# Kernel optimization log

Measured on AMD Instinct MI355X. Metric: run time of the kernel, lower is better.

The kernel has to match this reference:

```python
import jax, jax.numpy as jnp
import numpy as np

LRELU = 0.2


def _gru(x, Wi, Wh, bi, bh):
    # x: [B,T,D]; Wi: [3H,D]; Wh: [3H,H]; PyTorch GRU equations.
    B, T, D = x.shape
    H = Wh.shape[1]
    xW = jnp.einsum('btd,gd->btg', x, Wi) + bi  # precompute input projections
    def step(h, xw):
        gh = h @ Wh.T + bh
        xr, xz, xn = jnp.split(xw, 3, axis=-1)
        hr, hz, hn = jnp.split(gh, 3, axis=-1)
        r = jax.nn.sigmoid(xr + hr)
        z = jax.nn.sigmoid(xz + hz)
        n = jnp.tanh(xn + r * hn)
        h_new = (1.0 - z) * n + z * h
        return h_new, h_new
    h0 = jnp.zeros((B, H), x.dtype)
    hT, hs = jax.lax.scan(step, h0, jnp.swapaxes(xW, 0, 1))
    return jnp.swapaxes(hs, 0, 1), hT


def _gatv2(x, W, b, a, bias):
    # x: [B,N,F]; W: [2F,E]; lin([v_i||v_j]) == x_i@W1 + x_j@W2 + b (avoids materializing concat)
    F = x.shape[-1]
    W1, W2 = W[:F], W[F:]
    g1 = x @ W1            # [B,N,E]
    g2 = x @ W2 + b        # [B,N,E]
    z = jax.nn.leaky_relu(g1[:, :, None, :] + g2[:, None, :, :], LRELU)  # [B,N,N,E]
    e = jnp.einsum('bije,e->bij', z, a) + bias
    att = jax.nn.softmax(e, axis=2)
    return jax.nn.sigmoid(jnp.einsum('bij,bjf->bif', att, x))


def setup_inputs() -> dict:
    B, W, K, H, KS = 16, 256, 64, 150, 7
    key = jax.random.key(0)
    ks = jax.random.split(key, 32)
    def rn(i, sh, scale):
        return jax.random.normal(ks[i], sh, jnp.float32) * scale
    inp = {}
    inp['x'] = jax.random.normal(ks[0], (B, W, K), jnp.float32)
    inp['conv_w'] = rn(1, (K, K, KS), 1.0 / np.sqrt(K * KS))
    inp['conv_b'] = rn(2, (K,), 0.02)
    inp['fW'] = rn(3, (2 * W, 2 * W), 1.0 / np.sqrt(2 * W))
    inp['fb'] = rn(4, (2 * W,), 0.02)
    inp['fa'] = rn(5, (2 * W,), 1.0 / np.sqrt(2 * W))
    inp['fbias'] = rn(6, (K, K), 0.02)
    inp['tW'] = rn(7, (2 * K, 2 * K), 1.0 / np.sqrt(2 * K))
    inp['tb'] = rn(8, (2 * K,), 0.02)
    inp['ta'] = rn(9, (2 * K,), 1.0 / np.sqrt(2 * K))
    inp['tbias'] = rn(10, (W, W), 0.02)
    inp['gWi'] = rn(11, (3 * H, 3 * K), 1.0 / np.sqrt(H))
    inp['gWh'] = rn(12, (3 * H, H), 1.0 / np.sqrt(H))
    inp['gbi'] = rn(13, (3 * H,), 0.02)
    inp['gbh'] = rn(14, (3 * H,), 0.02)
    inp['f0w'] = rn(15, (H, H), 1.0 / np.sqrt(H))
    inp['f0b'] = rn(16, (H,), 0.02)
    inp['f1w'] = rn(17, (H, K), 1.0 / np.sqrt(H))
    inp['f1b'] = rn(18, (K,), 0.02)
    inp['rWi'] = rn(19, (3 * H, H), 1.0 / np.sqrt(H))
    inp['rWh'] = rn(20, (3 * H, H), 1.0 / np.sqrt(H))
    inp['rbi'] = rn(21, (3 * H,), 0.02)
    inp['rbh'] = rn(22, (3 * H,), 0.02)
    inp['rfw'] = rn(23, (H, K), 1.0 / np.sqrt(H))
    inp['rfb'] = rn(24, (K,), 0.02)
    return inp


def reference(x, conv_w, conv_b, fW, fb, fa, fbias, tW, tb, ta, tbias,
              gWi, gWh, gbi, gbh, f0w, f0b, f1w, f1b,
              rWi, rWh, rbi, rbh, rfw, rfb):
    B, Wsz, K = x.shape
    pad = (conv_w.shape[2] - 1) // 2
    # ConvLayer: permute -> constant pad -> conv1d -> relu -> permute back
    x_ncw = jnp.swapaxes(x, 1, 2)  # [B,K,W]
    x_pad = jnp.pad(x_ncw, ((0, 0), (0, 0), (pad, pad)))
    xc = jax.lax.conv_general_dilated(x_pad, conv_w, (1,), 'VALID',
                                      dimension_numbers=('NCW', 'OIW', 'NCW'))
    xc = jax.nn.relu(xc + conv_b[None, :, None])
    xc = jnp.swapaxes(xc, 1, 2)  # [B,W,K]
    # Feature GAT over nodes (K), temporal GAT over time (W)
    h_feat = jnp.swapaxes(_gatv2(jnp.swapaxes(xc, 1, 2), fW, fb, fa, fbias), 1, 2)  # [B,W,K]
    h_temp = _gatv2(xc, tW, tb, ta, tbias)  # [B,W,K]
    h_cat = jnp.concatenate([xc, h_feat, h_temp], axis=2)  # [B,W,3K]
    _, h_end = _gru(h_cat, gWi, gWh, gbi, gbh)  # [B,H]
    # Forecasting MLP (n_layers=1 -> two Linear layers)
    predictions = jax.nn.relu(h_end @ f0w + f0b) @ f1w + f1b  # [B,K]
    # Reconstruction: repeat_interleave over dim 1 then view(B, W, -1)
    H = h_end.shape[1]
    h_rep = jnp.repeat(h_end, Wsz, axis=1).reshape(B, Wsz, H)
    dec_out, _ = _gru(h_rep, rWi, rWh, rbi, rbh)  # [B,W,H]
    recons = dec_out @ rfw + rfb  # [B,W,K]
    return predictions, recons
```

## Files before the change

### kernel.cpp

```cpp
#include <hip/hip_runtime.h>
#include <hip/hip_fp16.h>

typedef _Float16 h2f __attribute__((ext_vector_type(2)));

__device__ __forceinline__ float dot2f(unsigned a, unsigned b, float c) {
#if __has_builtin(__builtin_amdgcn_fdot2)
  return __builtin_amdgcn_fdot2(__builtin_bit_cast(h2f, a),
                                __builtin_bit_cast(h2f, b), c, false);
#else
  h2f x = __builtin_bit_cast(h2f, a);
  h2f y = __builtin_bit_cast(h2f, b);
  return c + (float)x[0] * (float)y[0] + (float)x[1] * (float)y[1];
#endif
}

__device__ __forceinline__ float sigf(float x) { return 1.0f / (1.0f + __expf(-x)); }
__device__ __forceinline__ float tanhfast(float x) {
  float e = __expf(-2.0f * fabsf(x));
  float r = (1.0f - e) / (1.0f + e);
  return (x < 0.0f) ? -r : r;
}
__device__ __forceinline__ float lrelu(float x) { return x > 0.0f ? x : 0.2f * x; }

__global__ void k_prep(const float* __restrict__ conv_w, const float* __restrict__ gWi,
                       const float* __restrict__ gWh, const float* __restrict__ rWh,
                       const float* __restrict__ rWi,
                       float* __restrict__ cwT, float* __restrict__ gWiT,
                       unsigned* __restrict__ gWhP, unsigned* __restrict__ rWhP,
                       float* __restrict__ pref) {
  const int N0 = 64 * 64 * 7;
  const int N1 = 192 * 450;
  const int N2 = 76 * 450;
  const int N3 = 76 * 450;
  const int N4 = 450;
  int total = N0 + N1 + N2 + N3 + N4;
  for (int idx = blockIdx.x * blockDim.x + threadIdx.x; idx < total;
       idx += gridDim.x * blockDim.x) {
    if (idx < N0) {
      int k = idx & 63; int is = idx >> 6; int i = is / 7; int s = is - i * 7;
      cwT[idx] = conv_w[(k * 64 + i) * 7 + s];
    } else if (idx < N0 + N1) {
      int j = idx - N0; int g = j % 450; int d = j / 450;
      gWiT[j] = gWi[g * 192 + d];
    } else if (idx < N0 + N1 + N2) {
      int j = idx - (N0 + N1); int g = j % 450; int jj = j / 450;
      int j0 = 2 * jj, j1 = 2 * jj + 1;
      float a = (j0 < 150) ? gWh[g * 150 + j0] : 0.f;
      float b = (j1 < 150) ? gWh[g * 150 + j1] : 0.f;
      __half2 h = __floats2half2_rn(a, b);
      gWhP[j] = *reinterpret_cast<unsigned*>(&h);
    } else if (idx < N0 + N1 + N2 + N3) {
      int j = idx - (N0 + N1 + N2); int g = j % 450; int jj = j / 450;
      int j0 = 2 * jj, j1 = 2 * jj + 1;
      float a = (j0 < 150) ? rWh[g * 150 + j0] : 0.f;
      float b = (j1 < 150) ? rWh[g * 150 + j1] : 0.f;
      __half2 h = __floats2half2_rn(a, b);
      rWhP[j] = *reinterpret_cast<unsigned*>(&h);
    } else {
      int g = idx - (N0 + N1 + N2 + N3);
      float run = 0.f;
      pref[g] = 0.f;
      for (int j = 0; j < 150; ++j) { run += rWi[g * 150 + j]; pref[(j + 1) * 450 + g] = run; }
    }
  }
}

__global__ __launch_bounds__(256) void k_conv(const float* __restrict__ x,
                                              const float* __restrict__ cwT,
                                              const float* __restrict__ conv_b,
                                              float* __restrict__ xc) {
  __shared__ float xs[22 * 64];
  int b = blockIdx.y, t0 = blockIdx.x * 16, tid = threadIdx.x;
  for (int l = tid; l < 22 * 64; l += 256) {
    int r = l >> 6, i = l & 63;
    int t = t0 - 3 + r;
    xs[l] = (t >= 0 && t < 256) ? x[(b * 256 + t) * 64 + i] : 0.f;
  }
  __syncthreads();
  int k = tid & 63, tg = tid >> 6;
  float bias = conv_b[k];
  float acc[4] = {bias, bias, bias, bias};
  for (int i = 0; i < 64; ++i) {
#pragma unroll
    for (int s = 0; s < 7; ++s) {
      float wv = cwT[(i * 7 + s) * 64 + k];
#pragma unroll
      for (int q = 0; q < 4; ++q)
        acc[q] += xs[(tg * 4 + q + s) * 64 + i] * wv;
    }
  }
#pragma unroll
  for (int q = 0; q < 4; ++q)
    xc[(b * 256 + t0 + tg * 4 + q) * 64 + k] = fmaxf(acc[q], 0.f);
}

__global__ __launch_bounds__(512) void k_featg(const float* __restrict__ xc,
                                               const float* __restrict__ fW,
                                               const float* __restrict__ fb,
                                               float* __restrict__ g1f,
                                               float* __restrict__ g2fT) {
  __shared__ float xsL[256 * 8];
  int b = blockIdx.y, i0 = blockIdx.x * 8, e = threadIdx.x;
  for (int l = e; l < 2048; l += 512) {
    int t = l >> 3, ii = l & 7;
    xsL[l] = xc[(b * 256 + t) * 64 + i0 + ii];
  }
  __syncthreads();
  float a1[8] = {}, a2[8] = {};
  for (int t = 0; t < 256; ++t) {
    float w1 = fW[t * 512 + e];
    float w2 = fW[(256 + t) * 512 + e];
#pragma unroll
    for (int ii = 0; ii < 8; ++ii) {
      float s = xsL[t * 8 + ii];
      a1[ii] += s * w1; a2[ii] += s * w2;
    }
  }
  float fbe = fb[e];
#pragma unroll
  for (int ii = 0; ii < 8; ++ii)
    g1f[(b * 64 + i0 + ii) * 512 + e] = a1[ii];
  float4 v0 = make_float4(a2[0] + fbe, a2[1] + fbe, a2[2] + fbe, a2[3] + fbe);
  float4 v1 = make_float4(a2[4] + fbe, a2[5] + fbe, a2[6] + fbe, a2[7] + fbe);
  float4* p = reinterpret_cast<float4*>(&g2fT[(b * 512 + e) * 64 + i0]);
  p[0] = v0; p[1] = v1;
}

__global__ __launch_bounds__(256) void k_feata(const float* __restrict__ xc,
                                               const float* __restrict__ g1f,
                                               const float* __restrict__ g2fT,
                                               const float* __restrict__ fa,
                                               const float* __restrict__ fbias,
                                               float* __restrict__ h_feat) {
  __shared__ float g1L[512], faL[512], part[4 * 64], attL[64];
  int b = blockIdx.y, i = blockIdx.x, tid = threadIdx.x;
  for (int l = tid; l < 512; l += 256) {
    g1L[l] = g1f[(b * 64 + i) * 512 + l];
    faL[l] = fa[l];
  }
  __syncthreads();
  int q = tid >> 6, j = tid & 63;
  float acc = 0.f;
  for (int e = q * 128; e < q * 128 + 128; ++e) {
    float z = g1L[e] + g2fT[(b * 512 + e) * 64 + j];
    acc += faL[e] * lrelu(z);
  }
  part[q * 64 + j] = acc;
  __syncthreads();
  if (tid < 64) {
    float ev = part[tid] + part[64 + tid] + part[128 + tid] + part[192 + tid] +
               fbias[i * 64 + tid];
    float m = ev;
#pragma unroll
    for (int off = 32; off > 0; off >>= 1) m = fmaxf(m, __shfl_xor(m, off));
    float p = __expf(ev - m);
    float s = p;
#pragma unroll
    for (int off = 32; off > 0; off >>= 1) s += __shfl_xor(s, off);
    attL[tid] = p / s;
  }
  __syncthreads();
  float o = 0.f;
  for (int jj = 0; jj < 64; ++jj)
    o += attL[jj] * xc[(b * 256 + tid) * 64 + jj];
  h_feat[(b * 256 + tid) * 64 + i] = sigf(o);
}

__global__ __launch_bounds__(256) void k_tempg(const float* __restrict__ xc,
                                               const float* __restrict__ tW,
                                               const float* __restrict__ tb,
                                               float* __restrict__ g1t,
                                               float* __restrict__ g2tT) {
  __shared__ float xsL[16 * 64];
  int b = blockIdx.y, t0 = blockIdx.x * 16, tid = threadIdx.x;
  int e = tid & 127, th = tid >> 7;
  for (int l = tid; l < 1024; l += 256)
    xsL[l] = xc[(b * 256 + t0) * 64 + l];
  __syncthreads();
  float a1[8] = {}, a2[8] = {};
  for (int k = 0; k < 64; ++k) {
    float w1 = tW[k * 128 + e];
    float w2 = tW[(64 + k) * 128 + e];
#pragma unroll
    for (int tt = 0; tt < 8; ++tt) {
      float s = xsL[(th * 8 + tt) * 64 + k];
      a1[tt] += s * w1; a2[tt] += s * w2;
    }
  }
  float tbe = tb[e];
#pragma unroll
  for (int tt = 0; tt < 8; ++tt)
    g1t[(b * 256 + t0 + th * 8 + tt) * 128 + e] = a1[tt];
  float4 v0 = make_float4(a2[0] + tbe, a2[1] + tbe, a2[2] + tbe, a2[3] + tbe);
  float4 v1 = make_float4(a2[4] + tbe, a2[5] + tbe, a2[6] + tbe, a2[7] + tbe);
  float4* p = reinterpret_cast<float4*>(&g2tT[(b * 128 + e) * 256 + t0 + th * 8]);
  p[0] = v0; p[1] = v1;
}

__global__ __launch_bounds__(256) void k_tempa(const float* __restrict__ xc,
                                               const float* __restrict__ g1t,
                                               const float* __restrict__ g2tT,
                                               const float* __restrict__ ta,
                                               const float* __restrict__ tbias,
                                               float* __restrict__ h_temp) {
  __shared__ float g1L[4 * 128], taL[128], eL[4 * 256];
  int b = blockIdx.y, i0 = blockIdx.x * 4, tid = threadIdx.x;
  for (int l = tid; l < 512; l += 256)
    g1L[l] = g1t[(b * 256 + i0) * 128 + l];
  if (tid < 128) taL[tid] = ta[tid];
  __syncthreads();
  float acc[4] = {};
  for (int e = 0; e < 128; ++e) {
    float g2 = g2tT[(b * 128 + e) * 256 + tid];
    float tae = taL[e];
#pragma unroll
    for (int ii = 0; ii < 4; ++ii)
      acc[ii] += tae * lrelu(g1L[ii * 128 + e] + g2);
  }
#pragma unroll
  for (int ii = 0; ii < 4; ++ii)
    eL[ii * 256 + tid] = acc[ii] + tbias[(i0 + ii) * 256 + tid];
  __syncthreads();
  int wv = tid >> 6, ln = tid & 63;
  {
    float v0 = eL[wv * 256 + ln], v1 = eL[wv * 256 + 64 + ln];
    float v2 = eL[wv * 256 + 128 + ln], v3 = eL[wv * 256 + 192 + ln];
    float m = fmaxf(fmaxf(v0, v1), fmaxf(v2, v3));
#pragma unroll
    for (int off = 32; off > 0; off >>= 1) m = fmaxf(m, __shfl_xor(m, off));
    float p0 = __expf(v0 - m), p1 = __expf(v1 - m);
    float p2 = __expf(v2 - m), p3 = __expf(v3 - m);
    float s = p0 + p1 + p2 + p3;
#pragma unroll
    for (int off = 32; off > 0; off >>= 1) s += __shfl_xor(s, off);
    float rs = 1.f / s;
    eL[wv * 256 + ln] = p0 * rs; eL[wv * 256 + 64 + ln] = p1 * rs;
    eL[wv * 256 + 128 + ln] = p2 * rs; eL[wv * 256 + 192 + ln] = p3 * rs;
  }
  __syncthreads();
  int ii = tid >> 6, k = tid & 63;
  float o = 0.f;
  for (int j = 0; j < 256; ++j)
    o += eL[ii * 256 + j] * xc[(b * 256 + j) * 64 + k];
  h_temp[(b * 256 + i0 + ii) * 64 + k] = sigf(o);
}

__global__ __launch_bounds__(256) void k_xw(const float* __restrict__ xc,
                                            const float* __restrict__ h_feat,
                                            const float* __restrict__ h_temp,
                                            const float* __restrict__ gWiT,
                                            const float* __restrict__ gbi,
                                            float* __restrict__ xW) {
  __shared__ float hc[16 * 192];
  int b = blockIdx.z, t0 = blockIdx.y * 16, g0 = blockIdx.x * 128;
  int tid = threadIdx.x;
  for (int l = tid; l < 16 * 192; l += 256) {
    int tt = l / 192, d = l - tt * 192;
    int row = (b * 256 + t0 + tt) * 64;
    float v;
    if (d < 64) v = xc[row + d];
    else if (d < 128) v = h_feat[row + d - 64];
    else v = h_temp[row + d - 128];
    hc[l] = v;
  }
  __syncthreads();
  int gl = tid & 127, th = tid >> 7;
  int g = g0 + gl;
  if (g < 450) {
    float acc[8] = {};
    for (int d = 0; d < 192; ++d) {
      float w = gWiT[d * 450 + g];
#pragma unroll
      for (int tt = 0; tt < 8; ++tt)
        acc[tt] += hc[(th * 8 + tt) * 192 + d] * w;
    }
    float bi = gbi[g];
#pragma unroll
    for (int tt = 0; tt < 8; ++tt)
      xW[(b * 256 + t0 + th * 8 + tt) * 450 + g] = acc[tt] + bi;
  }
}

__global__ __launch_bounds__(512) void k_xwdec(const float* __restrict__ h_end,
                                               const float* __restrict__ pref,
                                               const float* __restrict__ rbi,
                                               float* __restrict__ xwD) {
  __shared__ float heL[160];
  int b = blockIdx.y, t0 = blockIdx.x * 16, g = threadIdx.x;
  if (g < 160) heL[g] = (g < 150) ? h_end[b * 150 + g] : 0.f;
  __syncthreads();
  if (g < 450) {
    float tot = pref[150 * 450 + g];
    float bi = rbi[g];
#pragma unroll 4
    for (int tt = 0; tt < 16; ++tt) {
      int t = t0 + tt;
      int base = 150 * t;
      int a = base >> 8;
      int c = 256 * (a + 1) - base; if (c > 150) c = 150;
      float pv = pref[c * 450 + g];
      xwD[(b * 256 + t) * 450 + g] = bi + heL[a] * pv + heL[a + 1] * (tot - pv);
    }
  }
}

__global__ __launch_bounds__(512) void k_gru(const float* __restrict__ xwAll,
                                             const unsigned* __restrict__ WhP,
                                             const float* __restrict__ bh,
                                             float* __restrict__ h_end,
                                             float* __restrict__ dec_out,
                                             int mode) {
  __shared__ __align__(16) unsigned hPair[80];
  __shared__ float hL32[152], rL[152], zL[152];
  int b = blockIdx.x, tid = threadIdx.x;
  if (tid < 80) hPair[tid] = 0u;
  if (tid < 152) hL32[tid] = 0.f;
  unsigned w[76];
  float bhv = 0.f;
  if (tid < 450) {
#pragma unroll
    for (int jj = 0; jj < 76; ++jj) w[jj] = WhP[jj * 450 + tid];
    bhv = bh[tid];
  }
  const float* xwrow = xwAll + (size_t)(b * 256) * 450;
  __syncthreads();
  const uint4* hp4 = reinterpret_cast<const uint4*>(hPair);
  for (int t = 0; t < 256; ++t) {
    float xwv = 0.f, acc = bhv;
    if (tid < 450) {
      xwv = xwrow[t * 450 + tid];
      float acc2 = 0.f;
#pragma unroll
      for (int q = 0; q < 19; ++q) {
        uint4 hv = hp4[q];
        acc  = dot2f(hv.x, w[4 * q + 0], acc);
        acc2 = dot2f(hv.y, w[4 * q + 1], acc2);
        acc  = dot2f(hv.z, w[4 * q + 2], acc);
        acc2 = dot2f(hv.w, w[4 * q + 3], acc2);
      }
      acc += acc2;
    }
    if (tid < 150) rL[tid] = sigf(xwv + acc);
    else if (tid < 300) zL[tid - 150] = sigf(xwv + acc);
    __syncthreads();
    if (tid >= 300 && tid < 450) {
      int i2 = tid - 300;
      float n = tanhfast(xwv + rL[i2] * acc);
      float z = zL[i2];
      float hn = (1.f - z) * n + z * hL32[i2];
      hL32[i2] = hn;
      reinterpret_cast<__half*>(hPair)[i2] = __float2half(hn);
      if (mode == 1) dec_out[((size_t)(b * 256) + t) * 150 + i2] = hn;
    }
    __syncthreads();
  }
  if (mode == 0 && tid < 150) h_end[b * 150 + tid] = hL32[tid];
}

__global__ __launch_bounds__(192) void k_pred(const float* __restrict__ h_end,
                                              const float* __restrict__ f0w,
                                              const float* __restrict__ f0b,
                                              const float* __restrict__ f1w,
                                              const float* __restrict__ f1b,
                                              float* __restrict__ out) {
  __shared__ float heL[152], t1L[152];
  int b = blockIdx.x, tid = threadIdx.x;
  if (tid < 152) heL[tid] = (tid < 150) ? h_end[b * 150 + tid] : 0.f;
  __syncthreads();
  if (tid < 150) {
    float a = f0b[tid];
    for (int i = 0; i < 150; ++i) a += heL[i] * f0w[i * 150 + tid];
    t1L[tid] = fmaxf(a, 0.f);
  }
  if (tid >= 150 && tid < 152) t1L[tid] = 0.f;
  __syncthreads();
  if (tid < 64) {
    float a = f1b[tid];
    for (int j = 0; j < 150; ++j) a += t1L[j] * f1w[j * 64 + tid];
    out[b * 64 + tid] = a;
  }
}

__global__ __launch_bounds__(256) void k_recon(const float* __restrict__ dec_out,
                                               const float* __restrict__ rfw,
                                               const float* __restrict__ rfb,
                                               float* __restrict__ out) {
  int row = blockIdx.x * 4 + (threadIdx.x >> 6);
  int k = threadIdx.x & 63;
  const float* d = dec_out + (size_t)row * 150;
  float a = rfb[k];
  for (int j = 0; j < 150; ++j) a += d[j] * rfw[j * 64 + k];
  out[1024 + (size_t)row * 64 + k] = a;
}

extern "C" void kernel_launch(void* const* d_in, const int* in_sizes, int n_in,
                              void* d_out, int out_size, void* d_ws, size_t ws_size,
                              hipStream_t stream) {
  (void)in_sizes; (void)n_in; (void)out_size; (void)ws_size;
  const float* x      = (const float*)d_in[0];
  const float* conv_w = (const float*)d_in[1];
  const float* conv_b = (const float*)d_in[2];
  const float* fW     = (const float*)d_in[3];
  const float* fb     = (const float*)d_in[4];
  const float* fa     = (const float*)d_in[5];
  const float* fbias  = (const float*)d_in[6];
  const float* tW     = (const float*)d_in[7];
  const float* tb     = (const float*)d_in[8];
  const float* ta     = (const float*)d_in[9];
  const float* tbias  = (const float*)d_in[10];
  const float* gWi    = (const float*)d_in[11];
  const float* gWh    = (const float*)d_in[12];
  const float* gbi    = (const float*)d_in[13];
  const float* gbh    = (const float*)d_in[14];
  const float* f0w    = (const float*)d_in[15];
  const float* f0b    = (const float*)d_in[16];
  const float* f1w    = (const float*)d_in[17];
  const float* f1b    = (const float*)d_in[18];
  const float* rWi    = (const float*)d_in[19];
  const float* rWh    = (const float*)d_in[20];
  const float* rbi    = (const float*)d_in[21];
  const float* rbh    = (const float*)d_in[22];
  const float* rfw    = (const float*)d_in[23];
  const float* rfb    = (const float*)d_in[24];
  float* out = (float*)d_out;
  float* ws  = (float*)d_ws;

  float* XC   = ws;
  float* HF   = XC + 262144;
  float* HT   = HF + 262144;
  float* GBUF = HT + 262144;
  float* G1F  = GBUF;
  float* G2FT = GBUF + 524288;
  float* G1T  = GBUF + 1048576;
  float* G2TT = GBUF + 1572864;
  float* XW   = GBUF;
  float* XWD  = GBUF;
  float* HEND = GBUF + 2097152;
  float* DEC  = HEND + 2400;
  float* CWT  = DEC + 614400;
  float* GWIT = CWT + 28672;
  unsigned* GWHP = (unsigned*)(GWIT + 86400);
  unsigned* RWHP = GWHP + 34200;
  float* PREF = (float*)(RWHP + 34200);

  k_prep<<<512, 256, 0, stream>>>(conv_w, gWi, gWh, rWh, rWi, CWT, GWIT, GWHP, RWHP, PREF);
  k_conv<<<dim3(16, 16), 256, 0, stream>>>(x, CWT, conv_b, XC);
  k_featg<<<dim3(8, 16), 512, 0, stream>>>(XC, fW, fb, G1F, G2FT);
  k_tempg<<<dim3(16, 16), 256, 0, stream>>>(XC, tW, tb, G1T, G2TT);
  k_feata<<<dim3(64, 16), 256, 0, stream>>>(XC, G1F, G2FT, fa, fbias, HF);
  k_tempa<<<dim3(64, 16), 256, 0, stream>>>(XC, G1T, G2TT, ta, tbias, HT);
  k_xw<<<dim3(4, 16, 16), 256, 0, stream>>>(XC, HF, HT, GWIT, gbi, XW);
  k_gru<<<16, 512, 0, stream>>>(XW, GWHP, gbh, HEND, nullptr, 0);
  k_pred<<<16, 192, 0, stream>>>(HEND, f0w, f0b, f1w, f1b, out);
  k_xwdec<<<dim3(16, 16), 512, 0, stream>>>(HEND, PREF, rbi, XWD);
  k_gru<<<16, 512, 0, stream>>>(XWD, RWHP, rbh, nullptr, DEC, 1);
  k_recon<<<1024, 256, 0, stream>>>(DEC, rfw, rfb, out);
}
```

Measured before the change: 619.7 us.

## Fuse decoder input projection into GRU kernel and prefetch inputs two steps ahead

The separate k_xwdec kernel is removed. The decoder GRU now computes its input projection on the fly from the prefix table and h_end, which saves one launch and a round trip of a [16,256,450] buffer through memory. Each step's input load is also prefetched two timesteps ahead to hide global-memory latency inside the serial recurrence, and the dot-product accumulators are split into four independent chains. A launch_bounds occupancy hint is added, which could limit registers available for the 76-entry weight array.

```diff
diff --git a/kernel.cpp b/kernel.cpp
--- a/kernel.cpp
+++ b/kernel.cpp
@@ -281,37 +281,17 @@
   }
 }
 
-__global__ __launch_bounds__(512) void k_xwdec(const float* __restrict__ h_end,
-                                               const float* __restrict__ pref,
-                                               const float* __restrict__ rbi,
-                                               float* __restrict__ xwD) {
-  __shared__ float heL[160];
-  int b = blockIdx.y, t0 = blockIdx.x * 16, g = threadIdx.x;
-  if (g < 160) heL[g] = (g < 150) ? h_end[b * 150 + g] : 0.f;
-  __syncthreads();
-  if (g < 450) {
-    float tot = pref[150 * 450 + g];
-    float bi = rbi[g];
-#pragma unroll 4
-    for (int tt = 0; tt < 16; ++tt) {
-      int t = t0 + tt;
-      int base = 150 * t;
-      int a = base >> 8;
-      int c = 256 * (a + 1) - base; if (c > 150) c = 150;
-      float pv = pref[c * 450 + g];
-      xwD[(b * 256 + t) * 450 + g] = bi + heL[a] * pv + heL[a + 1] * (tot - pv);
-    }
-  }
-}
-
-__global__ __launch_bounds__(512) void k_gru(const float* __restrict__ xwAll,
-                                             const unsigned* __restrict__ WhP,
-                                             const float* __restrict__ bh,
-                                             float* __restrict__ h_end,
-                                             float* __restrict__ dec_out,
-                                             int mode) {
+__global__ __launch_bounds__(512, 2) void k_gru(const float* __restrict__ xwAll,
+                                                const unsigned* __restrict__ WhP,
+                                                const float* __restrict__ bh,
+                                                const float* __restrict__ pref,
+                                                const float* __restrict__ rbi,
+                                                const float* __restrict__ h_end_in,
+                                                float* __restrict__ h_end,
+                                                float* __restrict__ dec_out,
+                                                int mode) {
   __shared__ __align__(16) unsigned hPair[80];
-  __shared__ float hL32[152], rL[152], zL[152];
+  __shared__ float hL32[152], rL[152], zL[152], heL[152];
   int b = blockIdx.x, tid = threadIdx.x;
   if (tid < 80) hPair[tid] = 0u;
   if (tid < 152) hL32[tid] = 0.f;
@@ -323,22 +303,47 @@
     bhv = bh[tid];
   }
   const float* xwrow = xwAll + (size_t)(b * 256) * 450;
-  __syncthreads();
+  float tot = 0.f, bi = 0.f;
+  if (mode == 1) {
+    if (tid < 152) heL[tid] = (tid < 150) ? h_end_in[b * 150 + tid] : 0.f;
+    if (tid < 450) { tot = pref[150 * 450 + tid]; bi = rbi[tid]; }
+  }
+  __syncthreads();
+
+  auto ldraw = [&](int t) -> float {
+    if (mode == 0) return xwrow[t * 450 + tid];
+    int base = 150 * t; int a = base >> 8;
+    int c = 256 * (a + 1) - base; if (c > 150) c = 150;
+    return pref[c * 450 + tid];
+  };
+
   const uint4* hp4 = reinterpret_cast<const uint4*>(hPair);
+  float r0 = 0.f, r1 = 0.f;
+  if (tid < 450) { r0 = ldraw(0); r1 = ldraw(1); }
+
   for (int t = 0; t < 256; ++t) {
-    float xwv = 0.f, acc = bhv;
+    float rf = 0.f;
+    if (tid < 450 && t + 2 < 256) rf = ldraw(t + 2);
+    float a0 = bhv, a1 = 0.f, a2 = 0.f, a3 = 0.f;
     if (tid < 450) {
-      xwv = xwrow[t * 450 + tid];
-      float acc2 = 0.f;
 #pragma unroll
       for (int q = 0; q < 19; ++q) {
         uint4 hv = hp4[q];
-        acc  = dot2f(hv.x, w[4 * q + 0], acc);
-        acc2 = dot2f(hv.y, w[4 * q + 1], acc2);
-        acc  = dot2f(hv.z, w[4 * q + 2], acc);
-        acc2 = dot2f(hv.w, w[4 * q + 3], acc2);
+        a0 = dot2f(hv.x, w[4 * q + 0], a0);
+        a1 = dot2f(hv.y, w[4 * q + 1], a1);
+        a2 = dot2f(hv.z, w[4 * q + 2], a2);
+        a3 = dot2f(hv.w, w[4 * q + 3], a3);
       }
-      acc += acc2;
+    }
+    float acc = (a0 + a1) + (a2 + a3);
+    float xwv = 0.f;
+    if (tid < 450) {
+      if (mode == 0) {
+        xwv = r0;
+      } else {
+        int base = 150 * t; int a = base >> 8;
+        xwv = bi + heL[a] * r0 + heL[a + 1] * (tot - r0);
+      }
     }
     if (tid < 150) rL[tid] = sigf(xwv + acc);
     else if (tid < 300) zL[tid - 150] = sigf(xwv + acc);
@@ -353,6 +358,7 @@
       if (mode == 1) dec_out[((size_t)(b * 256) + t) * 150 + i2] = hn;
     }
     __syncthreads();
+    r0 = r1; r1 = rf;
   }
   if (mode == 0 && tid < 150) h_end[b * 150 + tid] = hL32[tid];
 }
@@ -434,7 +440,6 @@
   float* G1T  = GBUF + 1048576;
   float* G2TT = GBUF + 1572864;
   float* XW   = GBUF;
-  float* XWD  = GBUF;
   float* HEND = GBUF + 2097152;
   float* DEC  = HEND + 2400;
   float* CWT  = DEC + 614400;
@@ -450,9 +455,8 @@
   k_feata<<<dim3(64, 16), 256, 0, stream>>>(XC, G1F, G2FT, fa, fbias, HF);
   k_tempa<<<dim3(64, 16), 256, 0, stream>>>(XC, G1T, G2TT, ta, tbias, HT);
   k_xw<<<dim3(4, 16, 16), 256, 0, stream>>>(XC, HF, HT, GWIT, gbi, XW);
-  k_gru<<<16, 512, 0, stream>>>(XW, GWHP, gbh, HEND, nullptr, 0);
+  k_gru<<<16, 512, 0, stream>>>(XW, GWHP, gbh, nullptr, nullptr, nullptr, HEND, nullptr, 0);
   k_pred<<<16, 192, 0, stream>>>(HEND, f0w, f0b, f1w, f1b, out);
-  k_xwdec<<<dim3(16, 16), 512, 0, stream>>>(HEND, PREF, rbi, XWD);
-  k_gru<<<16, 512, 0, stream>>>(XWD, RWHP, rbh, nullptr, DEC, 1);
+  k_gru<<<16, 512, 0, stream>>>(nullptr, RWHP, rbh, PREF, rbi, HEND, nullptr, DEC, 1);
   k_recon<<<1024, 256, 0, stream>>>(DEC, rfw, rfb, out);
 }
```

Result: slower. 718.5 us (+15.9%).
